# Kernel optimization log

Measured on AMD Instinct MI355X. Metric: run time of the kernel, lower is better.

## Reference

```python
import jax, jax.numpy as jnp
import numpy as np

B, H, W, D, K = 32, 64, 64, 128, 1024

def setup_inputs() -> dict:
    key = jax.random.key(0)
    k1, k2 = jax.random.split(key)
    inputs = jax.random.normal(k1, (B, H, W, D), dtype=jnp.float32)
    embedding = jax.random.normal(k2, (D, K), dtype=jnp.float32)  # codebook, column per code
    return {"inputs": inputs, "embedding": embedding}

def reference(inputs, embedding):
    D_ = embedding.shape[0]
    x = inputs.reshape(-1, D_)                                  # [N, D]
    dist = (jnp.sum(x * x, axis=-1, keepdims=True)
            - 2.0 * (x @ embedding)
            + jnp.sum(embedding * embedding, axis=0, keepdims=True))  # [N, K]
    idx = jnp.argmax(-dist, axis=1).reshape(inputs.shape[:-1])  # [B, H, W]
    return embedding.T[idx]                                     # [B, H, W, D]
```

## Files before the change

kernel.cpp:

```cpp
#include <hip/hip_runtime.h>

#define KC 1024
#define DD 128
#define NT_COUNT (KC / 16)
#define RPB 64

typedef short bf16x8 __attribute__((ext_vector_type(8)));
typedef float f32x4  __attribute__((ext_vector_type(4)));

#define AS1 __attribute__((address_space(1)))
#define AS3 __attribute__((address_space(3)))

static __device__ __forceinline__ unsigned short f2bf(float f) {
    unsigned u = __float_as_uint(f);
    unsigned r = (u + 0x7fffu + ((u >> 16) & 1u)) >> 16;
    return (unsigned short)r;
}
static __device__ __forceinline__ float bf2f(unsigned short h) {
    return __uint_as_float(((unsigned)h) << 16);
}
static __device__ __forceinline__ void gl_lds16(const void* g, void* l) {
    __builtin_amdgcn_global_load_lds((const AS1 void*)g, (AS3 void*)l, 16, 0, 0);
}
static __device__ __forceinline__ void gl_lds4(const void* g, void* l) {
    __builtin_amdgcn_global_load_lds((const AS1 void*)g, (AS3 void*)l, 4, 0, 0);
}

__global__ __launch_bounds__(256) void vq_prep(const float* __restrict__ E,
                                               float* __restrict__ e2h,
                                               float* __restrict__ ET,
                                               unsigned short* __restrict__ Bpk) {
    __shared__ float T[16 * 129];
    const int nt  = blockIdx.x;
    const int tid = threadIdx.x;

    for (int i = tid; i < 16 * DD; i += 256) {
        int d  = i >> 4;
        int kk = i & 15;
        T[kk * 129 + d] = E[(size_t)d * KC + nt * 16 + kk];
    }
    __syncthreads();

    if (tid < 16) {
        float s = 0.f;
#pragma unroll 16
        for (int d = 0; d < DD; ++d) {
            float v = T[tid * 129 + d];
            s = fmaf(v, v, s);
        }
        e2h[nt * 16 + tid] = 512.0f - 0.5f * s;
    }

    for (int i = tid; i < 16 * DD; i += 256) {
        int kk = i >> 7;
        int d  = i & 127;
        ET[(size_t)(nt * 16 + kk) * DD + d] = T[kk * 129 + d];
    }

    {
        const int s    = tid >> 6;
        const int lane = tid & 63;
        const int kk   = lane & 15;
        const int d0   = s * 32 + (lane >> 4) * 8;
        bf16x8 hi, lo;
#pragma unroll
        for (int j = 0; j < 8; ++j) {
            float v = T[kk * 129 + d0 + j];
            unsigned short h = f2bf(v);
            hi[j] = (short)h;
            lo[j] = (short)f2bf(v - bf2f(h));
        }
        char* base = (char*)Bpk + (size_t)nt * 8192 + s * 1024 + lane * 16;
        *(bf16x8*)(base)        = hi;
        *(bf16x8*)(base + 4096) = lo;
    }
}

__global__ __launch_bounds__(64, 2) void vq_main(const float* __restrict__ X,
                                                 const float* __restrict__ e2h,
                                                 const float* __restrict__ ET,
                                                 const unsigned short* __restrict__ Bpk,
                                                 float* __restrict__ Out) {
    __shared__ __align__(16) char lds[2 * 8448];
    int* s_k1  = (int*)(lds);
    int* s_k2  = (int*)(lds + 256);
    int* s_win = (int*)(lds + 512);

    const int lane  = threadIdx.x;
    const int quad  = lane >> 4;
    const int n16   = lane & 15;
    const int wrow0 = blockIdx.x * RPB;
    const int lidx16 = lane * 16;
    const int lidx4  = lane * 4;

    bf16x8 ahi[4][4], alo[4][4];
#pragma unroll
    for (int t = 0; t < 4; ++t) {
#pragma unroll
        for (int s = 0; s < 4; ++s) {
            const int row = wrow0 + t * 16 + n16;
            const int d0  = s * 32 + quad * 8;
            const float4 p = *(const float4*)(X + (size_t)row * DD + d0);
            const float4 q = *(const float4*)(X + (size_t)row * DD + d0 + 4);
            float v[8] = {p.x, p.y, p.z, p.w, q.x, q.y, q.z, q.w};
#pragma unroll
            for (int j = 0; j < 8; ++j) {
                unsigned short h = f2bf(v[j]);
                ahi[t][s][j] = (short)h;
                alo[t][s][j] = (short)f2bf(v[j] - bf2f(h));
            }
        }
    }

    float p1[4][4], p2[4][4];
#pragma unroll
    for (int t = 0; t < 4; ++t)
#pragma unroll
        for (int r = 0; r < 4; ++r) { p1[t][r] = 0.0f; p2[t][r] = 0.0f; }

#define STAGE(NT, BOFF)                                                          \
    do {                                                                         \
        const char* g = (const char*)Bpk + (size_t)(NT) * 8192;                  \
        _Pragma("unroll")                                                        \
        for (int c = 0; c < 8; ++c)                                              \
            gl_lds16(g + c * 1024 + lidx16, lds + (BOFF) + c * 1024);            \
        gl_lds4(e2h + (NT) * 16 + n16, lds + (BOFF) + 8192);                     \
    } while (0)

#define TILE(NT, BOFF)                                                           \
    do {                                                                         \
        const char* l = lds + (BOFF);                                            \
        const bf16x8 bh0 = *(const bf16x8*)(l + 0 * 1024 + lidx16);              \
        const bf16x8 bh1 = *(const bf16x8*)(l + 1 * 1024 + lidx16);              \
        const bf16x8 bh2 = *(const bf16x8*)(l + 2 * 1024 + lidx16);              \
        const bf16x8 bh3 = *(const bf16x8*)(l + 3 * 1024 + lidx16);              \
        const bf16x8 bl0 = *(const bf16x8*)(l + 4 * 1024 + lidx16);              \
        const bf16x8 bl1 = *(const bf16x8*)(l + 5 * 1024 + lidx16);              \
        const bf16x8 bl2 = *(const bf16x8*)(l + 6 * 1024 + lidx16);              \
        const bf16x8 bl3 = *(const bf16x8*)(l + 7 * 1024 + lidx16);              \
        const float  ev  = *(const float*)(l + 8192 + lidx4);                    \
        const unsigned ntinv = (unsigned)(63 - (NT));                            \
        _Pragma("unroll")                                                        \
        for (int t = 0; t < 4; ++t) {                                            \
            f32x4 acc = {ev, ev, ev, ev};                                        \
            acc = __builtin_amdgcn_mfma_f32_16x16x32_bf16(ahi[t][0], bh0, acc, 0, 0, 0); \
            acc = __builtin_amdgcn_mfma_f32_16x16x32_bf16(ahi[t][1], bh1, acc, 0, 0, 0); \
            acc = __builtin_amdgcn_mfma_f32_16x16x32_bf16(ahi[t][2], bh2, acc, 0, 0, 0); \
            acc = __builtin_amdgcn_mfma_f32_16x16x32_bf16(ahi[t][3], bh3, acc, 0, 0, 0); \
            acc = __builtin_amdgcn_mfma_f32_16x16x32_bf16(alo[t][0], bh0, acc, 0, 0, 0); \
            acc = __builtin_amdgcn_mfma_f32_16x16x32_bf16(alo[t][1], bh1, acc, 0, 0, 0); \
            acc = __builtin_amdgcn_mfma_f32_16x16x32_bf16(alo[t][2], bh2, acc, 0, 0, 0); \
            acc = __builtin_amdgcn_mfma_f32_16x16x32_bf16(alo[t][3], bh3, acc, 0, 0, 0); \
            acc = __builtin_amdgcn_mfma_f32_16x16x32_bf16(ahi[t][0], bl0, acc, 0, 0, 0); \
            acc = __builtin_amdgcn_mfma_f32_16x16x32_bf16(ahi[t][1], bl1, acc, 0, 0, 0); \
            acc = __builtin_amdgcn_mfma_f32_16x16x32_bf16(ahi[t][2], bl2, acc, 0, 0, 0); \
            acc = __builtin_amdgcn_mfma_f32_16x16x32_bf16(ahi[t][3], bl3, acc, 0, 0, 0); \
            _Pragma("unroll")                                                    \
            for (int r = 0; r < 4; ++r) {                                        \
                float v = __uint_as_float((__float_as_uint(acc[r]) & ~63u) | ntinv); \
                float lo = fminf(p1[t][r], v);                                   \
                p1[t][r] = fmaxf(p1[t][r], v);                                   \
                p2[t][r] = fmaxf(p2[t][r], lo);                                  \
            }                                                                    \
        }                                                                        \
    } while (0)

    STAGE(0, 0);
    for (int nt = 0; nt < NT_COUNT; nt += 2) {
        STAGE(nt + 1, 8448);
        __builtin_amdgcn_s_waitcnt(3961);
        __builtin_amdgcn_sched_barrier(0);
        TILE(nt, 0);
        if (nt + 2 < NT_COUNT) {
            STAGE(nt + 2, 0);
            __builtin_amdgcn_s_waitcnt(3961);
        } else {
            __builtin_amdgcn_s_waitcnt(3952);
        }
        __builtin_amdgcn_sched_barrier(0);
        TILE(nt + 1, 8448);
    }
#undef STAGE
#undef TILE

#pragma unroll
    for (int t = 0; t < 4; ++t) {
#pragma unroll
        for (int r = 0; r < 4; ++r) {
            unsigned u1 = __float_as_uint(p1[t][r]);
            unsigned u2 = __float_as_uint(p2[t][r]);
            int k1 = (int)(63u - (u1 & 63u)) * 16 + n16;
            int k2 = (int)(63u - (u2 & 63u)) * 16 + n16;
            unsigned long long q1 =
                ((unsigned long long)(u1 & ~63u) << 32) | (unsigned)(1023 - k1);
            unsigned long long q2 =
                ((unsigned long long)(u2 & ~63u) << 32) | (unsigned)(1023 - k2);
#pragma unroll
            for (int m = 1; m < 16; m <<= 1) {
                unsigned long long o1 = __shfl_xor(q1, m, 64);
                unsigned long long o2 = __shfl_xor(q2, m, 64);
                unsigned long long lo = q1 < o1 ? q1 : o1;
                q1 = q1 > o1 ? q1 : o1;
                unsigned long long hi2 = q2 > o2 ? q2 : o2;
                q2 = lo > hi2 ? lo : hi2;
            }
            if (n16 == 0) {
                int row = t * 16 + quad * 4 + r;
                s_k1[row] = 1023 - (int)(q1 & 1023u);
                s_k2[row] = 1023 - (int)(q2 & 1023u);
            }
        }
    }
    __syncthreads();

    {
        const int k1 = s_k1[lane];
        const int k2 = s_k2[lane];
        const float* __restrict__ xrow = X + (size_t)(wrow0 + lane) * DD;
        const float* __restrict__ e1 = ET + (size_t)k1 * DD;
        const float* __restrict__ e2p = ET + (size_t)k2 * DD;
        double dot1 = 0.0, ee1 = 0.0, dot2 = 0.0, ee2 = 0.0;
#pragma unroll 4
        for (int d = 0; d < DD; ++d) {
            double xv = (double)xrow[d];
            double v1 = (double)e1[d];
            double v2 = (double)e2p[d];
            dot1 = fma(xv, v1, dot1);
            ee1  = fma(v1, v1, ee1);
            dot2 = fma(xv, v2, dot2);
            ee2  = fma(v2, v2, ee2);
        }
        double d1 = ee1 - 2.0 * dot1;
        double d2 = ee2 - 2.0 * dot2;
        s_win[lane] = (d2 < d1 || (d2 == d1 && k2 < k1)) ? k2 : k1;
    }
    __syncthreads();

    for (int i = lane; i < RPB * (DD / 4); i += 64) {
        const int row = i >> 5;
        const int d4  = i & 31;
        const float4 v = *(const float4*)(ET + (size_t)s_win[row] * DD + d4 * 4);
        *(float4*)(Out + (size_t)(wrow0 + row) * DD + d4 * 4) = v;
    }
}

extern "C" void kernel_launch(void* const* d_in, const int* in_sizes, int n_in,
                              void* d_out, int out_size, void* d_ws, size_t ws_size,
                              hipStream_t stream) {
    const float* X = (const float*)d_in[0];
    const float* E = (const float*)d_in[1];
    float* Out = (float*)d_out;

    float* e2h = (float*)d_ws;
    float* ET  = e2h + KC;
    unsigned short* Bpk = (unsigned short*)(ET + (size_t)KC * DD);

    const int N = in_sizes[0] / DD;

    hipLaunchKernelGGL(vq_prep, dim3(NT_COUNT), dim3(256), 0, stream, E, e2h, ET, Bpk);
    hipLaunchKernelGGL(vq_main, dim3(N / RPB), dim3(64), 0, stream,
                       X, e2h, ET, Bpk, Out);
}
```

Before: 234.9 us.

## Share codebook tiles across four waves per block with cooperative staging

The main kernel moves from one 64-row wave per block to four waves per 256-thread block over 128 rows. Each wave loads a quarter of every codebook tile into LDS, with a barrier per tile, so global and LDS traffic for the codebook is shared across four waves. Code norms are preloaded into LDS once, and each block starts its tile loop at a different phase to spread L2 access. The two MFMA accumulation chains are interleaved, and the fp64 refinement is split so each thread handles one candidate. This adds a block-wide barrier per tile and lowers per-wave register use in exchange for more waves per CU.

After: 239.3 us. Within noise of the previous version (+1.8%).

```diff
diff --git a/kernel.cpp b/kernel.cpp
--- a/kernel.cpp
+++ b/kernel.cpp
@@ -3,7 +3,7 @@
 #define KC 1024
 #define DD 128
 #define NT_COUNT (KC / 16)
-#define RPB 64
+#define RPB 128
 
 typedef short bf16x8 __attribute__((ext_vector_type(8)));
 typedef float f32x4  __attribute__((ext_vector_type(4)));
@@ -21,9 +21,6 @@
 }
 static __device__ __forceinline__ void gl_lds16(const void* g, void* l) {
     __builtin_amdgcn_global_load_lds((const AS1 void*)g, (AS3 void*)l, 16, 0, 0);
-}
-static __device__ __forceinline__ void gl_lds4(const void* g, void* l) {
-    __builtin_amdgcn_global_load_lds((const AS1 void*)g, (AS3 void*)l, 4, 0, 0);
 }
 
 __global__ __launch_bounds__(256) void vq_prep(const float* __restrict__ E,
@@ -76,26 +73,34 @@
     }
 }
 
-__global__ __launch_bounds__(64, 2) void vq_main(const float* __restrict__ X,
-                                                 const float* __restrict__ e2h,
-                                                 const float* __restrict__ ET,
-                                                 const unsigned short* __restrict__ Bpk,
-                                                 float* __restrict__ Out) {
-    __shared__ __align__(16) char lds[2 * 8448];
-    int* s_k1  = (int*)(lds);
-    int* s_k2  = (int*)(lds + 256);
-    int* s_win = (int*)(lds + 512);
-
-    const int lane  = threadIdx.x;
+__global__ __launch_bounds__(256, 4) void vq_main(const float* __restrict__ X,
+                                                  const float* __restrict__ e2h,
+                                                  const float* __restrict__ ET,
+                                                  const unsigned short* __restrict__ Bpk,
+                                                  float* __restrict__ Out) {
+    __shared__ __align__(16) char lds[24064];
+    float*  e2s   = (float*)(lds + 16384);
+    int*    s_k1  = (int*)(lds + 20480);
+    int*    s_k2  = (int*)(lds + 20992);
+    int*    s_win = (int*)(lds + 21504);
+    double* s_d   = (double*)(lds + 22016);
+
+    const int tid   = threadIdx.x;
+    const int wave  = tid >> 6;
+    const int lane  = tid & 63;
     const int quad  = lane >> 4;
     const int n16   = lane & 15;
-    const int wrow0 = blockIdx.x * RPB;
+    const int brow0 = blockIdx.x * RPB;
+    const int wrow0 = brow0 + wave * 32;
     const int lidx16 = lane * 16;
-    const int lidx4  = lane * 4;
-
-    bf16x8 ahi[4][4], alo[4][4];
-#pragma unroll
-    for (int t = 0; t < 4; ++t) {
+    const int wave2  = wave * 2;
+    const int phase  = blockIdx.x & 63;
+
+    for (int i = tid; i < KC; i += 256) e2s[i] = e2h[i];
+
+    bf16x8 ahi[2][4], alo[2][4];
+#pragma unroll
+    for (int t = 0; t < 2; ++t) {
 #pragma unroll
         for (int s = 0; s < 4; ++s) {
             const int row = wrow0 + t * 16 + n16;
@@ -112,79 +117,93 @@
         }
     }
 
-    float p1[4][4], p2[4][4];
-#pragma unroll
-    for (int t = 0; t < 4; ++t)
+    float p1[2][4], p2[2][4];
+#pragma unroll
+    for (int t = 0; t < 2; ++t)
 #pragma unroll
         for (int r = 0; r < 4; ++r) { p1[t][r] = 0.0f; p2[t][r] = 0.0f; }
 
-#define STAGE(NT, BOFF)                                                          \
+#define STAGE(NTP, BOFF)                                                         \
     do {                                                                         \
-        const char* g = (const char*)Bpk + (size_t)(NT) * 8192;                  \
-        _Pragma("unroll")                                                        \
-        for (int c = 0; c < 8; ++c)                                              \
-            gl_lds16(g + c * 1024 + lidx16, lds + (BOFF) + c * 1024);            \
-        gl_lds4(e2h + (NT) * 16 + n16, lds + (BOFF) + 8192);                     \
+        const char* g = (const char*)Bpk + (size_t)(NTP) * 8192                  \
+                        + wave2 * 1024 + lidx16;                                 \
+        gl_lds16(g,        lds + (BOFF) + wave2 * 1024);                         \
+        gl_lds16(g + 1024, lds + (BOFF) + wave2 * 1024 + 1024);                  \
     } while (0)
 
-#define TILE(NT, BOFF)                                                           \
+#define TILE(NTP, BOFF)                                                          \
     do {                                                                         \
         const char* l = lds + (BOFF);                                            \
+        const float ev = e2s[(NTP) * 16 + n16];                                  \
         const bf16x8 bh0 = *(const bf16x8*)(l + 0 * 1024 + lidx16);              \
         const bf16x8 bh1 = *(const bf16x8*)(l + 1 * 1024 + lidx16);              \
         const bf16x8 bh2 = *(const bf16x8*)(l + 2 * 1024 + lidx16);              \
         const bf16x8 bh3 = *(const bf16x8*)(l + 3 * 1024 + lidx16);              \
+        f32x4 acc0 = {ev, ev, ev, ev};                                           \
+        f32x4 acc1 = {ev, ev, ev, ev};                                           \
+        acc0 = __builtin_amdgcn_mfma_f32_16x16x32_bf16(ahi[0][0], bh0, acc0, 0, 0, 0); \
+        acc1 = __builtin_amdgcn_mfma_f32_16x16x32_bf16(ahi[1][0], bh0, acc1, 0, 0, 0); \
+        acc0 = __builtin_amdgcn_mfma_f32_16x16x32_bf16(ahi[0][1], bh1, acc0, 0, 0, 0); \
+        acc1 = __builtin_amdgcn_mfma_f32_16x16x32_bf16(ahi[1][1], bh1, acc1, 0, 0, 0); \
+        acc0 = __builtin_amdgcn_mfma_f32_16x16x32_bf16(ahi[0][2], bh2, acc0, 0, 0, 0); \
+        acc1 = __builtin_amdgcn_mfma_f32_16x16x32_bf16(ahi[1][2], bh2, acc1, 0, 0, 0); \
+        acc0 = __builtin_amdgcn_mfma_f32_16x16x32_bf16(ahi[0][3], bh3, acc0, 0, 0, 0); \
+        acc1 = __builtin_amdgcn_mfma_f32_16x16x32_bf16(ahi[1][3], bh3, acc1, 0, 0, 0); \
+        acc0 = __builtin_amdgcn_mfma_f32_16x16x32_bf16(alo[0][0], bh0, acc0, 0, 0, 0); \
+        acc1 = __builtin_amdgcn_mfma_f32_16x16x32_bf16(alo[1][0], bh0, acc1, 0, 0, 0); \
+        acc0 = __builtin_amdgcn_mfma_f32_16x16x32_bf16(alo[0][1], bh1, acc0, 0, 0, 0); \
+        acc1 = __builtin_amdgcn_mfma_f32_16x16x32_bf16(alo[1][1], bh1, acc1, 0, 0, 0); \
+        acc0 = __builtin_amdgcn_mfma_f32_16x16x32_bf16(alo[0][2], bh2, acc0, 0, 0, 0); \
+        acc1 = __builtin_amdgcn_mfma_f32_16x16x32_bf16(alo[1][2], bh2, acc1, 0, 0, 0); \
+        acc0 = __builtin_amdgcn_mfma_f32_16x16x32_bf16(alo[0][3], bh3, acc0, 0, 0, 0); \
+        acc1 = __builtin_amdgcn_mfma_f32_16x16x32_bf16(alo[1][3], bh3, acc1, 0, 0, 0); \
         const bf16x8 bl0 = *(const bf16x8*)(l + 4 * 1024 + lidx16);              \
         const bf16x8 bl1 = *(const bf16x8*)(l + 5 * 1024 + lidx16);              \
         const bf16x8 bl2 = *(const bf16x8*)(l + 6 * 1024 + lidx16);              \
         const bf16x8 bl3 = *(const bf16x8*)(l + 7 * 1024 + lidx16);              \
-        const float  ev  = *(const float*)(l + 8192 + lidx4);                    \
-        const unsigned ntinv = (unsigned)(63 - (NT));                            \
+        acc0 = __builtin_amdgcn_mfma_f32_16x16x32_bf16(ahi[0][0], bl0, acc0, 0, 0, 0); \
+        acc1 = __builtin_amdgcn_mfma_f32_16x16x32_bf16(ahi[1][0], bl0, acc1, 0, 0, 0); \
+        acc0 = __builtin_amdgcn_mfma_f32_16x16x32_bf16(ahi[0][1], bl1, acc0, 0, 0, 0); \
+        acc1 = __builtin_amdgcn_mfma_f32_16x16x32_bf16(ahi[1][1], bl1, acc1, 0, 0, 0); \
+        acc0 = __builtin_amdgcn_mfma_f32_16x16x32_bf16(ahi[0][2], bl2, acc0, 0, 0, 0); \
+        acc1 = __builtin_amdgcn_mfma_f32_16x16x32_bf16(ahi[1][2], bl2, acc1, 0, 0, 0); \
+        acc0 = __builtin_amdgcn_mfma_f32_16x16x32_bf16(ahi[0][3], bl3, acc0, 0, 0, 0); \
+        acc1 = __builtin_amdgcn_mfma_f32_16x16x32_bf16(ahi[1][3], bl3, acc1, 0, 0, 0); \
+        const unsigned ntinv = (unsigned)(63 - (NTP));                           \
         _Pragma("unroll")                                                        \
-        for (int t = 0; t < 4; ++t) {                                            \
-            f32x4 acc = {ev, ev, ev, ev};                                        \
-            acc = __builtin_amdgcn_mfma_f32_16x16x32_bf16(ahi[t][0], bh0, acc, 0, 0, 0); \
-            acc = __builtin_amdgcn_mfma_f32_16x16x32_bf16(ahi[t][1], bh1, acc, 0, 0, 0); \
-            acc = __builtin_amdgcn_mfma_f32_16x16x32_bf16(ahi[t][2], bh2, acc, 0, 0, 0); \
-            acc = __builtin_amdgcn_mfma_f32_16x16x32_bf16(ahi[t][3], bh3, acc, 0, 0, 0); \
-            acc = __builtin_amdgcn_mfma_f32_16x16x32_bf16(alo[t][0], bh0, acc, 0, 0, 0); \
-            acc = __builtin_amdgcn_mfma_f32_16x16x32_bf16(alo[t][1], bh1, acc, 0, 0, 0); \
-            acc = __builtin_amdgcn_mfma_f32_16x16x32_bf16(alo[t][2], bh2, acc, 0, 0, 0); \
-            acc = __builtin_amdgcn_mfma_f32_16x16x32_bf16(alo[t][3], bh3, acc, 0, 0, 0); \
-            acc = __builtin_amdgcn_mfma_f32_16x16x32_bf16(ahi[t][0], bl0, acc, 0, 0, 0); \
-            acc = __builtin_amdgcn_mfma_f32_16x16x32_bf16(ahi[t][1], bl1, acc, 0, 0, 0); \
-            acc = __builtin_amdgcn_mfma_f32_16x16x32_bf16(ahi[t][2], bl2, acc, 0, 0, 0); \
-            acc = __builtin_amdgcn_mfma_f32_16x16x32_bf16(ahi[t][3], bl3, acc, 0, 0, 0); \
-            _Pragma("unroll")                                                    \
-            for (int r = 0; r < 4; ++r) {                                        \
-                float v = __uint_as_float((__float_as_uint(acc[r]) & ~63u) | ntinv); \
-                float lo = fminf(p1[t][r], v);                                   \
-                p1[t][r] = fmaxf(p1[t][r], v);                                   \
-                p2[t][r] = fmaxf(p2[t][r], lo);                                  \
-            }                                                                    \
+        for (int r = 0; r < 4; ++r) {                                            \
+            float v0 = __uint_as_float((__float_as_uint(acc0[r]) & ~63u) | ntinv); \
+            float l0 = fminf(p1[0][r], v0);                                      \
+            p1[0][r] = fmaxf(p1[0][r], v0);                                      \
+            p2[0][r] = fmaxf(p2[0][r], l0);                                      \
+            float v1 = __uint_as_float((__float_as_uint(acc1[r]) & ~63u) | ntinv); \
+            float l1 = fminf(p1[1][r], v1);                                      \
+            p1[1][r] = fmaxf(p1[1][r], v1);                                      \
+            p2[1][r] = fmaxf(p2[1][r], l1);                                      \
         }                                                                        \
     } while (0)
 
-    STAGE(0, 0);
-    for (int nt = 0; nt < NT_COUNT; nt += 2) {
-        STAGE(nt + 1, 8448);
-        __builtin_amdgcn_s_waitcnt(3961);
-        __builtin_amdgcn_sched_barrier(0);
-        TILE(nt, 0);
-        if (nt + 2 < NT_COUNT) {
-            STAGE(nt + 2, 0);
-            __builtin_amdgcn_s_waitcnt(3961);
-        } else {
+    STAGE(phase, 0);
+    __syncthreads();
+
+    for (int it = 0; it < NT_COUNT; ++it) {
+        const int boff = (it & 1) ? 8192 : 0;
+        if (it + 1 < NT_COUNT) {
+            STAGE((phase + it + 1) & 63, boff ^ 8192);
+        }
+        TILE((phase + it) & 63, boff);
+        if (it + 1 < NT_COUNT) {
             __builtin_amdgcn_s_waitcnt(3952);
-        }
-        __builtin_amdgcn_sched_barrier(0);
-        TILE(nt + 1, 8448);
+            __builtin_amdgcn_sched_barrier(0);
+            __builtin_amdgcn_s_barrier();
+            __builtin_amdgcn_sched_barrier(0);
+        }
     }
 #undef STAGE
 #undef TILE
 
 #pragma unroll
-    for (int t = 0; t < 4; ++t) {
+    for (int t = 0; t < 2; ++t) {
 #pragma unroll
         for (int r = 0; r < 4; ++r) {
             unsigned u1 = __float_as_uint(p1[t][r]);
@@ -205,7 +224,7 @@
                 q2 = lo > hi2 ? lo : hi2;
             }
             if (n16 == 0) {
-                int row = t * 16 + quad * 4 + r;
+                int row = wave * 32 + t * 16 + quad * 4 + r;
                 s_k1[row] = 1023 - (int)(q1 & 1023u);
                 s_k2[row] = 1023 - (int)(q2 & 1023u);
             }
@@ -214,33 +233,34 @@
     __syncthreads();
 
     {
-        const int k1 = s_k1[lane];
-        const int k2 = s_k2[lane];
-        const float* __restrict__ xrow = X + (size_t)(wrow0 + lane) * DD;
-        const float* __restrict__ e1 = ET + (size_t)k1 * DD;
-        const float* __restrict__ e2p = ET + (size_t)k2 * DD;
-        double dot1 = 0.0, ee1 = 0.0, dot2 = 0.0, ee2 = 0.0;
-#pragma unroll 4
+        const int row = tid >> 1;
+        const int k   = (tid & 1) ? s_k2[row] : s_k1[row];
+        const float* __restrict__ xrow = X + (size_t)(brow0 + row) * DD;
+        const float* __restrict__ erow = ET + (size_t)k * DD;
+        double dot = 0.0, ee = 0.0;
+#pragma unroll 8
         for (int d = 0; d < DD; ++d) {
             double xv = (double)xrow[d];
-            double v1 = (double)e1[d];
-            double v2 = (double)e2p[d];
-            dot1 = fma(xv, v1, dot1);
-            ee1  = fma(v1, v1, ee1);
-            dot2 = fma(xv, v2, dot2);
-            ee2  = fma(v2, v2, ee2);
-        }
-        double d1 = ee1 - 2.0 * dot1;
-        double d2 = ee2 - 2.0 * dot2;
-        s_win[lane] = (d2 < d1 || (d2 == d1 && k2 < k1)) ? k2 : k1;
-    }
-    __syncthreads();
-
-    for (int i = lane; i < RPB * (DD / 4); i += 64) {
+            double evd = (double)erow[d];
+            dot = fma(xv, evd, dot);
+            ee  = fma(evd, evd, ee);
+        }
+        s_d[tid] = ee - 2.0 * dot;
+    }
+    __syncthreads();
+    if (tid < RPB) {
+        double d1 = s_d[2 * tid];
+        double d2 = s_d[2 * tid + 1];
+        int kk1 = s_k1[tid], kk2 = s_k2[tid];
+        s_win[tid] = (d2 < d1 || (d2 == d1 && kk2 < kk1)) ? kk2 : kk1;
+    }
+    __syncthreads();
+
+    for (int i = tid; i < RPB * (DD / 4); i += 256) {
         const int row = i >> 5;
         const int d4  = i & 31;
         const float4 v = *(const float4*)(ET + (size_t)s_win[row] * DD + d4 * 4);
-        *(float4*)(Out + (size_t)(wrow0 + row) * DD + d4 * 4) = v;
+        *(float4*)(Out + (size_t)(brow0 + row) * DD + d4 * 4) = v;
     }
 }
 
@@ -258,6 +278,6 @@
     const int N = in_sizes[0] / DD;
 
     hipLaunchKernelGGL(vq_prep, dim3(NT_COUNT), dim3(256), 0, stream, E, e2h, ET, Bpk);
-    hipLaunchKernelGGL(vq_main, dim3(N / RPB), dim3(64), 0, stream,
+    hipLaunchKernelGGL(vq_main, dim3(N / RPB), dim3(256), 0, stream,
                        X, e2h, ET, Bpk, Out);
 }
```
